# Optimization experiments

Hardware: AMD Instinct MI355X
Metric: run time of the kernel (lower is better)

The kernel has to match this reference:

```python
import jax, jax.numpy as jnp
import numpy as np

N_NODES = 50000
N_EDGES = 800000
DIM = 256


def setup_inputs() -> dict:
    key = jax.random.key(0)
    k1, k2, k3, k4 = jax.random.split(key, 4)
    x = jax.random.normal(k1, (N_NODES, DIM), dtype=jnp.float32)
    edge_index = jax.random.randint(k2, (2, N_EDGES), 0, N_NODES, dtype=jnp.int64)
    # GCNConv learned params (glorot-style weight, zero bias like PyG default init)
    W = jax.random.normal(k3, (DIM, DIM), dtype=jnp.float32) * (1.0 / np.sqrt(DIM))
    b = jnp.zeros((DIM,), dtype=jnp.float32)
    return {"x": x, "edge_index": edge_index, "W": W, "b": b}


def reference(x, edge_index, W, b):
    # GNNBlock forward (eval mode: dropout is identity; normalizer=Identity,
    # activation=ReLU, projection=Identity since in_dim==out_dim).
    n = x.shape[0]
    # --- GCNConv with self-loops and symmetric normalization ---
    loop = jnp.arange(n, dtype=edge_index.dtype)
    src = jnp.concatenate([edge_index[0], loop])  # [E+N]
    dst = jnp.concatenate([edge_index[1], loop])  # [E+N]
    ones = jnp.ones(src.shape[0], dtype=x.dtype)
    deg = jax.ops.segment_sum(ones, dst, num_segments=n)  # in-degree incl. self-loop
    dinv = jnp.where(deg > 0, jax.lax.rsqrt(deg), 0.0)
    norm = dinv[src] * dinv[dst]  # [E+N]
    h = x @ W  # transform first (in->out), then aggregate
    msg = h[src] * norm[:, None]  # gather + scale, [E+N, DIM]
    agg = jax.ops.segment_sum(msg, dst, num_segments=n) + b  # scatter-add
    # --- norm (Identity) -> activation (ReLU) -> residual -> dropout (eval) ---
    out = jax.nn.relu(agg) + x
    return out
```

## Files before the change

### kernel.cpp

```cpp
#include <hip/hip_runtime.h>

#define N_NODES 50000
#define DIM 256
#define NBUCK 196
#define BCAP 6144
#define CEDGES 2048
#define APAD 264
#define EPAD 260

typedef __attribute__((ext_vector_type(8))) short bf16x8;
typedef __attribute__((ext_vector_type(4))) float f32x4;
typedef __attribute__((ext_vector_type(2))) float f32x2;
union U16 { uint4 u; bf16x8 s; };

__device__ __forceinline__ unsigned short f2b(float f) {
    unsigned int u = __float_as_uint(f);
    return (unsigned short)((u + 0x7FFFu + ((u >> 16) & 1u)) >> 16);
}

__global__ __launch_bounds__(256) void prep_bin_kernel(const int* __restrict__ src,
                                                       const int* __restrict__ dst, int E,
                                                       int nCoarse,
                                                       int* __restrict__ bcur,
                                                       unsigned int* __restrict__ slab,
                                                       const float* __restrict__ W,
                                                       uint4* __restrict__ Bpack,
                                                       const float* __restrict__ x,
                                                       unsigned int* __restrict__ xq) {
    __shared__ int hist[NBUCK];
    __shared__ int scn[NBUCK];
    __shared__ int gbase[NBUCK];
    __shared__ int cur[NBUCK];
    __shared__ int s2[256];
    __shared__ unsigned int sorted[CEDGES];

    const int tid = threadIdx.x;

    if (blockIdx.x >= (unsigned)nCoarse) {
        int role = blockIdx.x - nCoarse;
        if (role < 32) {
            int gid  = role * 256 + tid;
            int lane = gid & 63;
            int u    = (gid >> 6) & 15;
            int ki   = gid >> 10;
            int n    = u * 16 + (lane & 15);
            int k0   = ki * 32 + (lane >> 4) * 8;
            unsigned int w[4];
            #pragma unroll
            for (int p = 0; p < 4; ++p) {
                unsigned int lo = f2b(W[(size_t)(k0 + 2 * p) * DIM + n]);
                unsigned int hi = f2b(W[(size_t)(k0 + 2 * p + 1) * DIM + n]);
                w[p] = lo | (hi << 16);
            }
            Bpack[gid] = make_uint4(w[0], w[1], w[2], w[3]);
        } else {
            int gid = (role - 32) * 256 + tid;
            float4 v = ((const float4*)x)[gid];
            int p = __builtin_amdgcn_cvt_pk_fp8_f32(v.x, v.y, 0, false);
            p     = __builtin_amdgcn_cvt_pk_fp8_f32(v.z, v.w, p, true);
            xq[gid] = (unsigned int)p;
        }
        return;
    }

    const int e0 = blockIdx.x * CEDGES;
    const int nE = min(CEDGES, E - e0);

    if (tid < NBUCK) hist[tid] = 0;
    __syncthreads();

    unsigned int pk[8];
    #pragma unroll
    for (int i = 0; i < 8; ++i) {
        int idx = i * 256 + tid;
        pk[i] = 0xFFFFFFFFu;
        if (idx < nE) {
            unsigned int s = (unsigned int)src[e0 + idx];
            unsigned int d = (unsigned int)dst[e0 + idx];
            pk[i] = (d << 16) | s;
            atomicAdd(&hist[d >> 8], 1);
        }
    }
    __syncthreads();

    int v = (tid < NBUCK) ? hist[tid] : 0;
    s2[tid] = v;
    __syncthreads();
    for (int off = 1; off < 256; off <<= 1) {
        int t = (tid >= off) ? s2[tid - off] : 0;
        __syncthreads();
        s2[tid] += t;
        __syncthreads();
    }
    if (tid < NBUCK) {
        scn[tid] = s2[tid] - v;
        cur[tid] = 0;
        gbase[tid] = (v > 0) ? atomicAdd(&bcur[tid], v) : 0;
    }
    __syncthreads();

    #pragma unroll
    for (int i = 0; i < 8; ++i) {
        if (pk[i] != 0xFFFFFFFFu) {
            int bkt = pk[i] >> 24;
            int p = scn[bkt] + atomicAdd(&cur[bkt], 1);
            sorted[p] = pk[i];
        }
    }
    __syncthreads();

    for (int i = tid; i < nE; i += 256) {
        unsigned int p = sorted[i];
        int bkt = p >> 24;
        int gpos = gbase[bkt] + (i - scn[bkt]);
        if (gpos < BCAP) slab[(size_t)bkt * BCAP + gpos] = p;
    }
}

__global__ __launch_bounds__(256) void fine_kernel(const int* __restrict__ bcnt,
                                                   const unsigned int* __restrict__ slab,
                                                   int* __restrict__ offs,
                                                   int* __restrict__ deg,
                                                   float* __restrict__ dinv,
                                                   int* __restrict__ csr_src) {
    __shared__ int red[256];
    __shared__ int hist[256];
    __shared__ int scn[256];
    __shared__ unsigned int stage[BCAP];

    const int tid = threadIdx.x;
    const int g = blockIdx.x;

    red[tid] = (tid < g) ? min(bcnt[tid], BCAP) : 0;
    __syncthreads();
    for (int off = 128; off > 0; off >>= 1) {
        if (tid < off) red[tid] += red[tid + off];
        __syncthreads();
    }
    const int base = red[0];
    const int cnt = min(bcnt[g], BCAP);

    hist[tid] = 0;
    __syncthreads();
    for (int i = tid; i < cnt; i += 256) {
        unsigned int p = slab[(size_t)g * BCAP + i];
        stage[i] = p;
        atomicAdd(&hist[(p >> 16) & 255], 1);
    }
    __syncthreads();

    int d = hist[tid];
    scn[tid] = d;
    __syncthreads();
    for (int off = 1; off < 256; off <<= 1) {
        int t = (tid >= off) ? scn[tid - off] : 0;
        __syncthreads();
        scn[tid] += t;
        __syncthreads();
    }
    int excl = scn[tid] - d;

    int node = g * 256 + tid;
    if (node < N_NODES) {
        offs[node] = base + excl;
        deg[node]  = d;
        dinv[node] = rsqrtf((float)(d + 1));
    }
    hist[tid] = excl;
    __syncthreads();

    for (int i = tid; i < cnt; i += 256) {
        unsigned int p = stage[i];
        int pos = atomicAdd(&hist[(p >> 16) & 255], 1);
        csr_src[base + pos] = (int)(p & 0xFFFFu);
    }
}

__global__ __launch_bounds__(256) void agg_q_kernel(const unsigned int* __restrict__ xq,
                                                    const int* __restrict__ offs,
                                                    const int* __restrict__ deg,
                                                    const int* __restrict__ csr_src,
                                                    const float* __restrict__ dinv,
                                                    ushort4* __restrict__ aggb) {
    int row  = blockIdx.x * 4 + (threadIdx.x >> 6);
    int lane = threadIdx.x & 63;
    if (row >= N_NODES) return;

    float di = dinv[row];
    unsigned int qself = xq[(size_t)row * 64 + lane];
    f32x2 lo = __builtin_amdgcn_cvt_pk_f32_fp8((int)qself, false);
    f32x2 hi = __builtin_amdgcn_cvt_pk_f32_fp8((int)qself, true);
    float ax = lo.x * di, ay = lo.y * di, az = hi.x * di, aw = hi.y * di;

    int start = offs[row];
    int n     = deg[row];
    int i = 0;
    for (; i + 8 <= n; i += 8) {
        int s0 = csr_src[start + i + 0], s1 = csr_src[start + i + 1];
        int s2 = csr_src[start + i + 2], s3 = csr_src[start + i + 3];
        int s4 = csr_src[start + i + 4], s5 = csr_src[start + i + 5];
        int s6 = csr_src[start + i + 6], s7 = csr_src[start + i + 7];
        unsigned int q0 = xq[(size_t)s0 * 64 + lane];
        unsigned int q1 = xq[(size_t)s1 * 64 + lane];
        unsigned int q2 = xq[(size_t)s2 * 64 + lane];
        unsigned int q3 = xq[(size_t)s3 * 64 + lane];
        unsigned int q4 = xq[(size_t)s4 * 64 + lane];
        unsigned int q5 = xq[(size_t)s5 * 64 + lane];
        unsigned int q6 = xq[(size_t)s6 * 64 + lane];
        unsigned int q7 = xq[(size_t)s7 * 64 + lane];
        float d0 = dinv[s0], d1 = dinv[s1], d2 = dinv[s2], d3 = dinv[s3];
        float d4 = dinv[s4], d5 = dinv[s5], d6 = dinv[s6], d7 = dinv[s7];
        #pragma unroll
        for (int u = 0; u < 8; ++u) {
            unsigned int q; float dd;
            switch (u) {
                case 0: q = q0; dd = d0; break; case 1: q = q1; dd = d1; break;
                case 2: q = q2; dd = d2; break; case 3: q = q3; dd = d3; break;
                case 4: q = q4; dd = d4; break; case 5: q = q5; dd = d5; break;
                case 6: q = q6; dd = d6; break; default: q = q7; dd = d7; break;
            }
            f32x2 l = __builtin_amdgcn_cvt_pk_f32_fp8((int)q, false);
            f32x2 h = __builtin_amdgcn_cvt_pk_f32_fp8((int)q, true);
            ax += l.x * dd; ay += l.y * dd; az += h.x * dd; aw += h.y * dd;
        }
    }
    for (; i < n; ++i) {
        int s = csr_src[start + i];
        unsigned int q = xq[(size_t)s * 64 + lane];
        float dd = dinv[s];
        f32x2 l = __builtin_amdgcn_cvt_pk_f32_fp8((int)q, false);
        f32x2 h = __builtin_amdgcn_cvt_pk_f32_fp8((int)q, true);
        ax += l.x * dd; ay += l.y * dd; az += h.x * dd; aw += h.y * dd;
    }
    ax *= di; ay *= di; az *= di; aw *= di;
    aggb[(size_t)row * 64 + lane] = make_ushort4(f2b(ax), f2b(ay), f2b(az), f2b(aw));
}

__global__ __launch_bounds__(256) void gemm_kernel(const uint4* __restrict__ aggb16,
                                                   const float* __restrict__ x,
                                                   const uint4* __restrict__ Bpack,
                                                   const float* __restrict__ b,
                                                   float* __restrict__ out) {
    __shared__ __align__(16) char LDSraw[64 * APAD * 2];
    ushort* ALDS = (ushort*)LDSraw;
    float*  ELDS = (float*)LDSraw;

    const int tid  = threadIdx.x;
    const int row0 = blockIdx.x * 64;

    #pragma unroll
    for (int i = 0; i < 8; ++i) {
        int c = i * 256 + tid;
        int r = c >> 5;
        int q = c & 31;
        int row = row0 + r;
        uint4 v = make_uint4(0, 0, 0, 0);
        if (row < N_NODES) v = aggb16[(size_t)row * 32 + q];
        *(uint4*)&ALDS[r * APAD + q * 8] = v;
    }
    __syncthreads();

    const int wave = tid >> 6;
    const int lane = tid & 63;
    const int m    = lane & 15;
    const int kb   = lane >> 4;

    f32x4 acc[4][4];
    #pragma unroll
    for (int t = 0; t < 4; ++t)
        #pragma unroll
        for (int r = 0; r < 4; ++r) acc[t][r] = (f32x4){0.f, 0.f, 0.f, 0.f};

    const uint4* bp = Bpack + (size_t)(wave * 4) * 64 + lane;

    for (int ki = 0; ki < 8; ++ki) {
        U16 bf[4], af[4];
        #pragma unroll
        for (int t = 0; t < 4; ++t) bf[t].u = bp[(size_t)(ki * 16 + t) * 64];
        #pragma unroll
        for (int r = 0; r < 4; ++r)
            af[r].u = *(const uint4*)&ALDS[(r * 16 + m) * APAD + ki * 32 + kb * 8];
        #pragma unroll
        for (int t = 0; t < 4; ++t)
            #pragma unroll
            for (int r = 0; r < 4; ++r)
                acc[t][r] = __builtin_amdgcn_mfma_f32_16x16x32_bf16(af[r].s, bf[t].s, acc[t][r], 0, 0, 0);
    }

    const float4* x4g = (const float4*)x;
    const float4* b4  = (const float4*)b;
    float4* out4 = (float4*)out;

    #pragma unroll
    for (int p = 0; p < 2; ++p) {
        __syncthreads();
        #pragma unroll
        for (int t = 0; t < 4; ++t) {
            #pragma unroll
            for (int rl = 0; rl < 2; ++rl) {
                int r = p * 2 + rl;
                #pragma unroll
                for (int reg = 0; reg < 4; ++reg) {
                    ELDS[(rl * 16 + kb * 4 + reg) * EPAD + wave * 64 + t * 16 + m] = acc[t][r][reg];
                }
            }
        }
        __syncthreads();
        #pragma unroll
        for (int j = 0; j < 8; ++j) {
            int idx  = j * 256 + tid;
            int lrow = idx >> 6;
            int c4   = idx & 63;
            int grow = row0 + p * 32 + lrow;
            if (grow < N_NODES) {
                float4 v  = *(const float4*)&ELDS[lrow * EPAD + c4 * 4];
                float4 bb = b4[c4];
                float4 xx = x4g[(size_t)grow * 64 + c4];
                float4 o;
                o.x = fmaxf(v.x + bb.x, 0.f) + xx.x;
                o.y = fmaxf(v.y + bb.y, 0.f) + xx.y;
                o.z = fmaxf(v.z + bb.z, 0.f) + xx.z;
                o.w = fmaxf(v.w + bb.w, 0.f) + xx.w;
                out4[(size_t)grow * 64 + c4] = o;
            }
        }
    }
}

extern "C" void kernel_launch(void* const* d_in, const int* in_sizes, int n_in,
                              void* d_out, int out_size, void* d_ws, size_t ws_size,
                              hipStream_t stream) {
    const float* x  = (const float*)d_in[0];
    const int*   ei = (const int*)d_in[1];
    const float* W  = (const float*)d_in[2];
    const float* b  = (const float*)d_in[3];
    float* out = (float*)d_out;
    const int E = in_sizes[1] / 2;

    char* ws = (char*)d_ws;
    int*          bcur    = (int*)(ws);
    int*          deg     = (int*)(ws + 4096);
    int*          offs    = (int*)(ws + 208896);
    float*        dinv    = (float*)(ws + 413696);
    int*          csr_src = (int*)(ws + 618496);
    unsigned int* slab    = (unsigned int*)(ws + 3821568);
    ushort4*      aggb    = (ushort4*)(ws + 8640512);
    uint4*        Bpack   = (uint4*)(ws + 34240512);
    unsigned int* xq      = (unsigned int*)(ws + 34371584);

    const int* src = ei;
    const int* dst = ei + E;

    hipMemsetAsync(bcur, 0, NBUCK * sizeof(int), stream);

    const int nCoarse = (E + CEDGES - 1) / CEDGES;
    const int nXq = (N_NODES * 64) / 256;
    prep_bin_kernel<<<nCoarse + 32 + nXq, 256, 0, stream>>>(src, dst, E, nCoarse,
                                                            bcur, slab, W, Bpack, x, xq);
    fine_kernel<<<NBUCK, 256, 0, stream>>>(bcur, slab, offs, deg, dinv, csr_src);
    agg_q_kernel<<<(N_NODES + 3) / 4, 256, 0, stream>>>(xq, offs, deg, csr_src, dinv, aggb);
    gemm_kernel<<<(N_NODES + 63) / 64, 256, 0, stream>>>((const uint4*)aggb, x, Bpack, b, out);
}
```

Baseline: 196.5 us.

## Fuse four kernels and memset into one persistent cooperative kernel with grid syncs

Replaces the memset plus four separate launches (prep/bin, fine CSR build, fp8 aggregation, bf16 MFMA GEMM) with a single cooperative persistent kernel. Blocks loop over work units in each phase, and grid.sync separates the phases. The aim is to remove launch gaps and per-kernel ramp-up and tail costs. In exchange, grid size is capped by occupancy, LDS is shared across phases, and grid-wide barriers are paid on every phase boundary.

```diff
diff --git a/kernel.cpp b/kernel.cpp
--- a/kernel.cpp
+++ b/kernel.cpp
@@ -1,4 +1,7 @@
 #include <hip/hip_runtime.h>
+#include <hip/hip_cooperative_groups.h>
+
+namespace cg = cooperative_groups;
 
 #define N_NODES 50000
 #define DIM 256
@@ -7,6 +10,7 @@
 #define CEDGES 2048
 #define APAD 264
 #define EPAD 260
+#define LDS_BYTES 33792
 
 typedef __attribute__((ext_vector_type(8))) short bf16x8;
 typedef __attribute__((ext_vector_type(4))) float f32x4;
@@ -18,310 +22,323 @@
     return (unsigned short)((u + 0x7FFFu + ((u >> 16) & 1u)) >> 16);
 }
 
-__global__ __launch_bounds__(256) void prep_bin_kernel(const int* __restrict__ src,
-                                                       const int* __restrict__ dst, int E,
-                                                       int nCoarse,
-                                                       int* __restrict__ bcur,
-                                                       unsigned int* __restrict__ slab,
-                                                       const float* __restrict__ W,
-                                                       uint4* __restrict__ Bpack,
-                                                       const float* __restrict__ x,
-                                                       unsigned int* __restrict__ xq) {
-    __shared__ int hist[NBUCK];
-    __shared__ int scn[NBUCK];
-    __shared__ int gbase[NBUCK];
-    __shared__ int cur[NBUCK];
-    __shared__ int s2[256];
-    __shared__ unsigned int sorted[CEDGES];
+__global__ __launch_bounds__(256, 4) void fused_kernel(
+        const int* __restrict__ src, const int* __restrict__ dst,
+        const int E, const int nCoarse,
+        int* __restrict__ bcur, unsigned int* __restrict__ slab,
+        const float* __restrict__ W, uint4* __restrict__ Bpack,
+        const float* __restrict__ x, unsigned int* __restrict__ xq,
+        int* __restrict__ offs, int* __restrict__ deg,
+        float* __restrict__ dinv, int* __restrict__ csr_src,
+        ushort4* __restrict__ aggb,
+        const float* __restrict__ b, float* __restrict__ out) {
+    cg::grid_group grid = cg::this_grid();
+    __shared__ __align__(16) char LDSraw[LDS_BYTES];
 
     const int tid = threadIdx.x;
-
-    if (blockIdx.x >= (unsigned)nCoarse) {
-        int role = blockIdx.x - nCoarse;
-        if (role < 32) {
-            int gid  = role * 256 + tid;
-            int lane = gid & 63;
-            int u    = (gid >> 6) & 15;
-            int ki   = gid >> 10;
-            int n    = u * 16 + (lane & 15);
-            int k0   = ki * 32 + (lane >> 4) * 8;
-            unsigned int w[4];
+    const int nb  = gridDim.x;
+
+    if (blockIdx.x == 0 && tid < NBUCK) bcur[tid] = 0;
+    __threadfence();
+    grid.sync();
+
+    {
+        int* hist  = (int*)LDSraw;
+        int* scn   = hist + NBUCK;
+        int* gbase = scn + NBUCK;
+        int* cur   = gbase + NBUCK;
+        int* s2    = cur + NBUCK;
+        unsigned int* sorted = (unsigned int*)(s2 + 256);
+
+        const int NU = nCoarse + 32 + (N_NODES * 64) / 256;
+        for (int u = blockIdx.x; u < NU; u += nb) {
+            if (u >= nCoarse) {
+                int role = u - nCoarse;
+                if (role < 32) {
+                    int gid  = role * 256 + tid;
+                    int lane = gid & 63;
+                    int uu   = (gid >> 6) & 15;
+                    int ki   = gid >> 10;
+                    int n    = uu * 16 + (lane & 15);
+                    int k0   = ki * 32 + (lane >> 4) * 8;
+                    unsigned int w[4];
+                    #pragma unroll
+                    for (int p = 0; p < 4; ++p) {
+                        unsigned int lo = f2b(W[(size_t)(k0 + 2 * p) * DIM + n]);
+                        unsigned int hi = f2b(W[(size_t)(k0 + 2 * p + 1) * DIM + n]);
+                        w[p] = lo | (hi << 16);
+                    }
+                    Bpack[gid] = make_uint4(w[0], w[1], w[2], w[3]);
+                } else {
+                    int gid = (role - 32) * 256 + tid;
+                    float4 v = ((const float4*)x)[gid];
+                    int p = __builtin_amdgcn_cvt_pk_fp8_f32(v.x, v.y, 0, false);
+                    p     = __builtin_amdgcn_cvt_pk_fp8_f32(v.z, v.w, p, true);
+                    xq[gid] = (unsigned int)p;
+                }
+                continue;
+            }
+
+            __syncthreads();
+            const int e0 = u * CEDGES;
+            const int nE = min(CEDGES, E - e0);
+
+            if (tid < NBUCK) hist[tid] = 0;
+            __syncthreads();
+
+            unsigned int pk[8];
             #pragma unroll
-            for (int p = 0; p < 4; ++p) {
-                unsigned int lo = f2b(W[(size_t)(k0 + 2 * p) * DIM + n]);
-                unsigned int hi = f2b(W[(size_t)(k0 + 2 * p + 1) * DIM + n]);
-                w[p] = lo | (hi << 16);
-            }
-            Bpack[gid] = make_uint4(w[0], w[1], w[2], w[3]);
-        } else {
-            int gid = (role - 32) * 256 + tid;
-            float4 v = ((const float4*)x)[gid];
-            int p = __builtin_amdgcn_cvt_pk_fp8_f32(v.x, v.y, 0, false);
-            p     = __builtin_amdgcn_cvt_pk_fp8_f32(v.z, v.w, p, true);
-            xq[gid] = (unsigned int)p;
+            for (int i = 0; i < 8; ++i) {
+                int idx = i * 256 + tid;
+                pk[i] = 0xFFFFFFFFu;
+                if (idx < nE) {
+                    unsigned int s = (unsigned int)src[e0 + idx];
+                    unsigned int d = (unsigned int)dst[e0 + idx];
+                    pk[i] = (d << 16) | s;
+                    atomicAdd(&hist[d >> 8], 1);
+                }
+            }
+            __syncthreads();
+
+            int v = (tid < NBUCK) ? hist[tid] : 0;
+            s2[tid] = v;
+            __syncthreads();
+            for (int off = 1; off < 256; off <<= 1) {
+                int t = (tid >= off) ? s2[tid - off] : 0;
+                __syncthreads();
+                s2[tid] += t;
+                __syncthreads();
+            }
+            if (tid < NBUCK) {
+                scn[tid] = s2[tid] - v;
+                cur[tid] = 0;
+                gbase[tid] = (v > 0) ? atomicAdd(&bcur[tid], v) : 0;
+            }
+            __syncthreads();
+
+            #pragma unroll
+            for (int i = 0; i < 8; ++i) {
+                if (pk[i] != 0xFFFFFFFFu) {
+                    int bkt = pk[i] >> 24;
+                    int p = scn[bkt] + atomicAdd(&cur[bkt], 1);
+                    sorted[p] = pk[i];
+                }
+            }
+            __syncthreads();
+
+            for (int i = tid; i < nE; i += 256) {
+                unsigned int p = sorted[i];
+                int bkt = p >> 24;
+                int gpos = gbase[bkt] + (i - scn[bkt]);
+                if (gpos < BCAP) slab[(size_t)bkt * BCAP + gpos] = p;
+            }
         }
-        return;
-    }
-
-    const int e0 = blockIdx.x * CEDGES;
-    const int nE = min(CEDGES, E - e0);
-
-    if (tid < NBUCK) hist[tid] = 0;
-    __syncthreads();
-
-    unsigned int pk[8];
-    #pragma unroll
-    for (int i = 0; i < 8; ++i) {
-        int idx = i * 256 + tid;
-        pk[i] = 0xFFFFFFFFu;
-        if (idx < nE) {
-            unsigned int s = (unsigned int)src[e0 + idx];
-            unsigned int d = (unsigned int)dst[e0 + idx];
-            pk[i] = (d << 16) | s;
-            atomicAdd(&hist[d >> 8], 1);
+    }
+    __threadfence();
+    grid.sync();
+
+    {
+        int* red  = (int*)LDSraw;
+        int* hist = red + 256;
+        int* scn  = hist + 256;
+        unsigned int* stage = (unsigned int*)(scn + 256);
+
+        for (int g = blockIdx.x; g < NBUCK; g += nb) {
+            __syncthreads();
+
+            red[tid] = (tid < g) ? min(bcur[tid], BCAP) : 0;
+            __syncthreads();
+            for (int off = 128; off > 0; off >>= 1) {
+                if (tid < off) red[tid] += red[tid + off];
+                __syncthreads();
+            }
+            const int base = red[0];
+            const int cnt = min(bcur[g], BCAP);
+
+            hist[tid] = 0;
+            __syncthreads();
+            for (int i = tid; i < cnt; i += 256) {
+                unsigned int p = slab[(size_t)g * BCAP + i];
+                stage[i] = p;
+                atomicAdd(&hist[(p >> 16) & 255], 1);
+            }
+            __syncthreads();
+
+            int d = hist[tid];
+            scn[tid] = d;
+            __syncthreads();
+            for (int off = 1; off < 256; off <<= 1) {
+                int t = (tid >= off) ? scn[tid - off] : 0;
+                __syncthreads();
+                scn[tid] += t;
+                __syncthreads();
+            }
+            int excl = scn[tid] - d;
+
+            int node = g * 256 + tid;
+            if (node < N_NODES) {
+                offs[node] = base + excl;
+                deg[node]  = d;
+                dinv[node] = rsqrtf((float)(d + 1));
+            }
+            hist[tid] = excl;
+            __syncthreads();
+
+            for (int i = tid; i < cnt; i += 256) {
+                unsigned int p = stage[i];
+                int pos = atomicAdd(&hist[(p >> 16) & 255], 1);
+                csr_src[base + pos] = (int)(p & 0xFFFFu);
+            }
         }
     }
-    __syncthreads();
-
-    int v = (tid < NBUCK) ? hist[tid] : 0;
-    s2[tid] = v;
-    __syncthreads();
-    for (int off = 1; off < 256; off <<= 1) {
-        int t = (tid >= off) ? s2[tid - off] : 0;
-        __syncthreads();
-        s2[tid] += t;
-        __syncthreads();
-    }
-    if (tid < NBUCK) {
-        scn[tid] = s2[tid] - v;
-        cur[tid] = 0;
-        gbase[tid] = (v > 0) ? atomicAdd(&bcur[tid], v) : 0;
-    }
-    __syncthreads();
-
-    #pragma unroll
-    for (int i = 0; i < 8; ++i) {
-        if (pk[i] != 0xFFFFFFFFu) {
-            int bkt = pk[i] >> 24;
-            int p = scn[bkt] + atomicAdd(&cur[bkt], 1);
-            sorted[p] = pk[i];
+    __threadfence();
+    grid.sync();
+
+    {
+        const int NU = (N_NODES + 3) / 4;
+        const int lane = tid & 63;
+        for (int uu = blockIdx.x; uu < NU; uu += nb) {
+            int row = uu * 4 + (tid >> 6);
+            if (row < N_NODES) {
+                float di = dinv[row];
+                unsigned int qself = xq[(size_t)row * 64 + lane];
+                f32x2 lo = __builtin_amdgcn_cvt_pk_f32_fp8((int)qself, false);
+                f32x2 hi = __builtin_amdgcn_cvt_pk_f32_fp8((int)qself, true);
+                float ax = lo.x * di, ay = lo.y * di, az = hi.x * di, aw = hi.y * di;
+
+                int start = offs[row];
+                int n     = deg[row];
+                int i = 0;
+                for (; i + 8 <= n; i += 8) {
+                    int s0 = csr_src[start + i + 0], s1 = csr_src[start + i + 1];
+                    int s2 = csr_src[start + i + 2], s3 = csr_src[start + i + 3];
+                    int s4 = csr_src[start + i + 4], s5 = csr_src[start + i + 5];
+                    int s6 = csr_src[start + i + 6], s7 = csr_src[start + i + 7];
+                    unsigned int q0 = xq[(size_t)s0 * 64 + lane];
+                    unsigned int q1 = xq[(size_t)s1 * 64 + lane];
+                    unsigned int q2 = xq[(size_t)s2 * 64 + lane];
+                    unsigned int q3 = xq[(size_t)s3 * 64 + lane];
+                    unsigned int q4 = xq[(size_t)s4 * 64 + lane];
+                    unsigned int q5 = xq[(size_t)s5 * 64 + lane];
+                    unsigned int q6 = xq[(size_t)s6 * 64 + lane];
+                    unsigned int q7 = xq[(size_t)s7 * 64 + lane];
+                    float d0 = dinv[s0], d1 = dinv[s1], d2 = dinv[s2], d3 = dinv[s3];
+                    float d4 = dinv[s4], d5 = dinv[s5], d6 = dinv[s6], d7 = dinv[s7];
+                    #pragma unroll
+                    for (int u2 = 0; u2 < 8; ++u2) {
+                        unsigned int q; float dd;
+                        switch (u2) {
+                            case 0: q = q0; dd = d0; break; case 1: q = q1; dd = d1; break;
+                            case 2: q = q2; dd = d2; break; case 3: q = q3; dd = d3; break;
+                            case 4: q = q4; dd = d4; break; case 5: q = q5; dd = d5; break;
+                            case 6: q = q6; dd = d6; break; default: q = q7; dd = d7; break;
+                        }
+                        f32x2 l = __builtin_amdgcn_cvt_pk_f32_fp8((int)q, false);
+                        f32x2 h = __builtin_amdgcn_cvt_pk_f32_fp8((int)q, true);
+                        ax += l.x * dd; ay += l.y * dd; az += h.x * dd; aw += h.y * dd;
+                    }
+                }
+                for (; i < n; ++i) {
+                    int s = csr_src[start + i];
+                    unsigned int q = xq[(size_t)s * 64 + lane];
+                    float dd = dinv[s];
+                    f32x2 l = __builtin_amdgcn_cvt_pk_f32_fp8((int)q, false);
+                    f32x2 h = __builtin_amdgcn_cvt_pk_f32_fp8((int)q, true);
+                    ax += l.x * dd; ay += l.y * dd; az += h.x * dd; aw += h.y * dd;
+                }
+                ax *= di; ay *= di; az *= di; aw *= di;
+                aggb[(size_t)row * 64 + lane] = make_ushort4(f2b(ax), f2b(ay), f2b(az), f2b(aw));
+            }
         }
     }
-    __syncthreads();
-
-    for (int i = tid; i < nE; i += 256) {
-        unsigned int p = sorted[i];
-        int bkt = p >> 24;
-        int gpos = gbase[bkt] + (i - scn[bkt]);
-        if (gpos < BCAP) slab[(size_t)bkt * BCAP + gpos] = p;
-    }
-}
-
-__global__ __launch_bounds__(256) void fine_kernel(const int* __restrict__ bcnt,
-                                                   const unsigned int* __restrict__ slab,
-                                                   int* __restrict__ offs,
-                                                   int* __restrict__ deg,
-                                                   float* __restrict__ dinv,
-                                                   int* __restrict__ csr_src) {
-    __shared__ int red[256];
-    __shared__ int hist[256];
-    __shared__ int scn[256];
-    __shared__ unsigned int stage[BCAP];
-
-    const int tid = threadIdx.x;
-    const int g = blockIdx.x;
-
-    red[tid] = (tid < g) ? min(bcnt[tid], BCAP) : 0;
-    __syncthreads();
-    for (int off = 128; off > 0; off >>= 1) {
-        if (tid < off) red[tid] += red[tid + off];
-        __syncthreads();
-    }
-    const int base = red[0];
-    const int cnt = min(bcnt[g], BCAP);
-
-    hist[tid] = 0;
-    __syncthreads();
-    for (int i = tid; i < cnt; i += 256) {
-        unsigned int p = slab[(size_t)g * BCAP + i];
-        stage[i] = p;
-        atomicAdd(&hist[(p >> 16) & 255], 1);
-    }
-    __syncthreads();
-
-    int d = hist[tid];
-    scn[tid] = d;
-    __syncthreads();
-    for (int off = 1; off < 256; off <<= 1) {
-        int t = (tid >= off) ? scn[tid - off] : 0;
-        __syncthreads();
-        scn[tid] += t;
-        __syncthreads();
-    }
-    int excl = scn[tid] - d;
-
-    int node = g * 256 + tid;
-    if (node < N_NODES) {
-        offs[node] = base + excl;
-        deg[node]  = d;
-        dinv[node] = rsqrtf((float)(d + 1));
-    }
-    hist[tid] = excl;
-    __syncthreads();
-
-    for (int i = tid; i < cnt; i += 256) {
-        unsigned int p = stage[i];
-        int pos = atomicAdd(&hist[(p >> 16) & 255], 1);
-        csr_src[base + pos] = (int)(p & 0xFFFFu);
-    }
-}
-
-__global__ __launch_bounds__(256) void agg_q_kernel(const unsigned int* __restrict__ xq,
-                                                    const int* __restrict__ offs,
-                                                    const int* __restrict__ deg,
-                                                    const int* __restrict__ csr_src,
-                                                    const float* __restrict__ dinv,
-                                                    ushort4* __restrict__ aggb) {
-    int row  = blockIdx.x * 4 + (threadIdx.x >> 6);
-    int lane = threadIdx.x & 63;
-    if (row >= N_NODES) return;
-
-    float di = dinv[row];
-    unsigned int qself = xq[(size_t)row * 64 + lane];
-    f32x2 lo = __builtin_amdgcn_cvt_pk_f32_fp8((int)qself, false);
-    f32x2 hi = __builtin_amdgcn_cvt_pk_f32_fp8((int)qself, true);
-    float ax = lo.x * di, ay = lo.y * di, az = hi.x * di, aw = hi.y * di;
-
-    int start = offs[row];
-    int n     = deg[row];
-    int i = 0;
-    for (; i + 8 <= n; i += 8) {
-        int s0 = csr_src[start + i + 0], s1 = csr_src[start + i + 1];
-        int s2 = csr_src[start + i + 2], s3 = csr_src[start + i + 3];
-        int s4 = csr_src[start + i + 4], s5 = csr_src[start + i + 5];
-        int s6 = csr_src[start + i + 6], s7 = csr_src[start + i + 7];
-        unsigned int q0 = xq[(size_t)s0 * 64 + lane];
-        unsigned int q1 = xq[(size_t)s1 * 64 + lane];
-        unsigned int q2 = xq[(size_t)s2 * 64 + lane];
-        unsigned int q3 = xq[(size_t)s3 * 64 + lane];
-        unsigned int q4 = xq[(size_t)s4 * 64 + lane];
-        unsigned int q5 = xq[(size_t)s5 * 64 + lane];
-        unsigned int q6 = xq[(size_t)s6 * 64 + lane];
-        unsigned int q7 = xq[(size_t)s7 * 64 + lane];
-        float d0 = dinv[s0], d1 = dinv[s1], d2 = dinv[s2], d3 = dinv[s3];
-        float d4 = dinv[s4], d5 = dinv[s5], d6 = dinv[s6], d7 = dinv[s7];
-        #pragma unroll
-        for (int u = 0; u < 8; ++u) {
-            unsigned int q; float dd;
-            switch (u) {
-                case 0: q = q0; dd = d0; break; case 1: q = q1; dd = d1; break;
-                case 2: q = q2; dd = d2; break; case 3: q = q3; dd = d3; break;
-                case 4: q = q4; dd = d4; break; case 5: q = q5; dd = d5; break;
-                case 6: q = q6; dd = d6; break; default: q = q7; dd = d7; break;
-            }
-            f32x2 l = __builtin_amdgcn_cvt_pk_f32_fp8((int)q, false);
-            f32x2 h = __builtin_amdgcn_cvt_pk_f32_fp8((int)q, true);
-            ax += l.x * dd; ay += l.y * dd; az += h.x * dd; aw += h.y * dd;
-        }
-    }
-    for (; i < n; ++i) {
-        int s = csr_src[start + i];
-        unsigned int q = xq[(size_t)s * 64 + lane];
-        float dd = dinv[s];
-        f32x2 l = __builtin_amdgcn_cvt_pk_f32_fp8((int)q, false);
-        f32x2 h = __builtin_amdgcn_cvt_pk_f32_fp8((int)q, true);
-        ax += l.x * dd; ay += l.y * dd; az += h.x * dd; aw += h.y * dd;
-    }
-    ax *= di; ay *= di; az *= di; aw *= di;
-    aggb[(size_t)row * 64 + lane] = make_ushort4(f2b(ax), f2b(ay), f2b(az), f2b(aw));
-}
-
-__global__ __launch_bounds__(256) void gemm_kernel(const uint4* __restrict__ aggb16,
-                                                   const float* __restrict__ x,
-                                                   const uint4* __restrict__ Bpack,
-                                                   const float* __restrict__ b,
-                                                   float* __restrict__ out) {
-    __shared__ __align__(16) char LDSraw[64 * APAD * 2];
-    ushort* ALDS = (ushort*)LDSraw;
-    float*  ELDS = (float*)LDSraw;
-
-    const int tid  = threadIdx.x;
-    const int row0 = blockIdx.x * 64;
-
-    #pragma unroll
-    for (int i = 0; i < 8; ++i) {
-        int c = i * 256 + tid;
-        int r = c >> 5;
-        int q = c & 31;
-        int row = row0 + r;
-        uint4 v = make_uint4(0, 0, 0, 0);
-        if (row < N_NODES) v = aggb16[(size_t)row * 32 + q];
-        *(uint4*)&ALDS[r * APAD + q * 8] = v;
-    }
-    __syncthreads();
-
-    const int wave = tid >> 6;
-    const int lane = tid & 63;
-    const int m    = lane & 15;
-    const int kb   = lane >> 4;
-
-    f32x4 acc[4][4];
-    #pragma unroll
-    for (int t = 0; t < 4; ++t)
-        #pragma unroll
-        for (int r = 0; r < 4; ++r) acc[t][r] = (f32x4){0.f, 0.f, 0.f, 0.f};
-
-    const uint4* bp = Bpack + (size_t)(wave * 4) * 64 + lane;
-
-    for (int ki = 0; ki < 8; ++ki) {
-        U16 bf[4], af[4];
-        #pragma unroll
-        for (int t = 0; t < 4; ++t) bf[t].u = bp[(size_t)(ki * 16 + t) * 64];
-        #pragma unroll
-        for (int r = 0; r < 4; ++r)
-            af[r].u = *(const uint4*)&ALDS[(r * 16 + m) * APAD + ki * 32 + kb * 8];
-        #pragma unroll
-        for (int t = 0; t < 4; ++t)
+    __threadfence();
+    grid.sync();
+
+    {
+        ushort* ALDS = (ushort*)LDSraw;
+        float*  ELDS = (float*)LDSraw;
+        const uint4* aggb16 = (const uint4*)aggb;
+        const int wave = tid >> 6;
+        const int lane = tid & 63;
+        const int m    = lane & 15;
+        const int kb   = lane >> 4;
+        const int NU = (N_NODES + 63) / 64;
+
+        for (int u = blockIdx.x; u < NU; u += nb) {
+            const int row0 = u * 64;
+            __syncthreads();
+
             #pragma unroll
-            for (int r = 0; r < 4; ++r)
-                acc[t][r] = __builtin_amdgcn_mfma_f32_16x16x32_bf16(af[r].s, bf[t].s, acc[t][r], 0, 0, 0);
-    }
-
-    const float4* x4g = (const float4*)x;
-    const float4* b4  = (const float4*)b;
-    float4* out4 = (float4*)out;
-
-    #pragma unroll
-    for (int p = 0; p < 2; ++p) {
-        __syncthreads();
-        #pragma unroll
-        for (int t = 0; t < 4; ++t) {
+            for (int i = 0; i < 8; ++i) {
+                int c = i * 256 + tid;
+                int r = c >> 5;
+                int q = c & 31;
+                int row = row0 + r;
+                uint4 v = make_uint4(0, 0, 0, 0);
+                if (row < N_NODES) v = aggb16[(size_t)row * 32 + q];
+                *(uint4*)&ALDS[r * APAD + q * 8] = v;
+            }
+            __syncthreads();
+
+            f32x4 acc[4][4];
             #pragma unroll
-            for (int rl = 0; rl < 2; ++rl) {
-                int r = p * 2 + rl;
-                #pragma unroll
-                for (int reg = 0; reg < 4; ++reg) {
-                    ELDS[(rl * 16 + kb * 4 + reg) * EPAD + wave * 64 + t * 16 + m] = acc[t][r][reg];
-                }
-            }
-        }
-        __syncthreads();
-        #pragma unroll
-        for (int j = 0; j < 8; ++j) {
-            int idx  = j * 256 + tid;
-            int lrow = idx >> 6;
-            int c4   = idx & 63;
-            int grow = row0 + p * 32 + lrow;
-            if (grow < N_NODES) {
-                float4 v  = *(const float4*)&ELDS[lrow * EPAD + c4 * 4];
-                float4 bb = b4[c4];
-                float4 xx = x4g[(size_t)grow * 64 + c4];
-                float4 o;
-                o.x = fmaxf(v.x + bb.x, 0.f) + xx.x;
-                o.y = fmaxf(v.y + bb.y, 0.f) + xx.y;
-                o.z = fmaxf(v.z + bb.z, 0.f) + xx.z;
-                o.w = fmaxf(v.w + bb.w, 0.f) + xx.w;
-                out4[(size_t)grow * 64 + c4] = o;
+            for (int t = 0; t < 4; ++t)
+                #pragma unroll
+                for (int r = 0; r < 4; ++r) acc[t][r] = (f32x4){0.f, 0.f, 0.f, 0.f};
+
+            const uint4* bp = Bpack + (size_t)(wave * 4) * 64 + lane;
+
+            for (int ki = 0; ki < 8; ++ki) {
+                U16 bf[4], af[4];
+                #pragma unroll
+                for (int t = 0; t < 4; ++t) bf[t].u = bp[(size_t)(ki * 16 + t) * 64];
+                #pragma unroll
+                for (int r = 0; r < 4; ++r)
+                    af[r].u = *(const uint4*)&ALDS[(r * 16 + m) * APAD + ki * 32 + kb * 8];
+                #pragma unroll
+                for (int t = 0; t < 4; ++t)
+                    #pragma unroll
+                    for (int r = 0; r < 4; ++r)
+                        acc[t][r] = __builtin_amdgcn_mfma_f32_16x16x32_bf16(af[r].s, bf[t].s, acc[t][r], 0, 0, 0);
+            }
+
+            const float4* x4g = (const float4*)x;
+            const float4* b4  = (const float4*)b;
+            float4* out4 = (float4*)out;
+
+            #pragma unroll
+            for (int p = 0; p < 2; ++p) {
+                __syncthreads();
+                #pragma unroll
+                for (int t = 0; t < 4; ++t) {
+                    #pragma unroll
+                    for (int rl = 0; rl < 2; ++rl) {
+                        int r = p * 2 + rl;
+                        #pragma unroll
+                        for (int reg = 0; reg < 4; ++reg) {
+                            ELDS[(rl * 16 + kb * 4 + reg) * EPAD + wave * 64 + t * 16 + m] = acc[t][r][reg];
+                        }
+                    }
+                }
+                __syncthreads();
+                #pragma unroll
+                for (int j = 0; j < 8; ++j) {
+                    int idx  = j * 256 + tid;
+                    int lrow = idx >> 6;
+                    int c4   = idx & 63;
+                    int grow = row0 + p * 32 + lrow;
+                    if (grow < N_NODES) {
+                        float4 v  = *(const float4*)&ELDS[lrow * EPAD + c4 * 4];
+                        float4 bb = b4[c4];
+                        float4 xx = x4g[(size_t)grow * 64 + c4];
+                        float4 o;
+                        o.x = fmaxf(v.x + bb.x, 0.f) + xx.x;
+                        o.y = fmaxf(v.y + bb.y, 0.f) + xx.y;
+                        o.z = fmaxf(v.z + bb.z, 0.f) + xx.z;
+                        o.w = fmaxf(v.w + bb.w, 0.f) + xx.w;
+                        out4[(size_t)grow * 64 + c4] = o;
+                    }
+                }
             }
         }
     }
@@ -350,14 +367,37 @@
 
     const int* src = ei;
     const int* dst = ei + E;
-
-    hipMemsetAsync(bcur, 0, NBUCK * sizeof(int), stream);
-
     const int nCoarse = (E + CEDGES - 1) / CEDGES;
-    const int nXq = (N_NODES * 64) / 256;
-    prep_bin_kernel<<<nCoarse + 32 + nXq, 256, 0, stream>>>(src, dst, E, nCoarse,
-                                                            bcur, slab, W, Bpack, x, xq);
-    fine_kernel<<<NBUCK, 256, 0, stream>>>(bcur, slab, offs, deg, dinv, csr_src);
-    agg_q_kernel<<<(N_NODES + 3) / 4, 256, 0, stream>>>(xq, offs, deg, csr_src, dinv, aggb);
-    gemm_kernel<<<(N_NODES + 63) / 64, 256, 0, stream>>>((const uint4*)aggb, x, Bpack, b, out);
+
+    static int s_nb = -1;
+    if (s_nb < 0) {
+        int maxB = 0;
+        hipOccupancyMaxActiveBlocksPerMultiprocessor(&maxB, fused_kernel, 256, 0);
+        if (maxB < 1) maxB = 1;
+        hipDeviceProp_t prop;
+        int dev = 0;
+        hipGetDevice(&dev);
+        hipGetDeviceProperties(&prop, dev);
+        long nb = (long)maxB * prop.multiProcessorCount;
+        if (nb > 2048) nb = 2048;
+        if (nb < NBUCK) nb = NBUCK;
+        s_nb = (int)nb;
+    }
+
+    {
+        const int* a_src = src; const int* a_dst = dst;
+        int a_E = E; int a_nC = nCoarse;
+        int* a_bcur = bcur; unsigned int* a_slab = slab;
+        const float* a_W = W; uint4* a_Bpack = Bpack;
+        const float* a_x = x; unsigned int* a_xq = xq;
+        int* a_offs = offs; int* a_deg = deg;
+        float* a_dinv = dinv; int* a_csr = csr_src;
+        ushort4* a_aggb = aggb;
+        const float* a_b = b; float* a_out = out;
+        void* args[] = {&a_src, &a_dst, &a_E, &a_nC, &a_bcur, &a_slab,
+                        &a_W, &a_Bpack, &a_x, &a_xq, &a_offs, &a_deg,
+                        &a_dinv, &a_csr, &a_aggb, &a_b, &a_out};
+        hipLaunchCooperativeKernel((void*)fused_kernel, dim3(s_nb), dim3(256),
+                                   args, 0, stream);
+    }
 }
```

Result: slower. 685.7 us (+248.9%).
